# Kernel tuning notes

Hardware: AMD Instinct MI355X
Metric: run time of the kernel (lower is better)

## Reference

```python
import jax, jax.numpy as jnp
import numpy as np

B, L, H, D = 8, 4800, 8, 64  # L = 60*80 tokens, D = head_dim = self.dim


def setup_inputs() -> dict:
    key = jax.random.key(0)
    ks = jax.random.split(key, 8)
    q = jax.random.normal(ks[0], (B, L, H, D), jnp.float32)
    k = jax.random.normal(ks[1], (B, L, H, D), jnp.float32)
    v = jax.random.normal(ks[2], (B, L, H, D), jnp.float32)
    temperature = jnp.ones((H, 1, 1), jnp.float32)          # nn.Parameter(torch.ones(H,1,1))
    attns = jnp.ones((4,), jnp.float32)                      # four scalar gate params (init 1.0)
    # Conv1d(dim,1,k=1): weight [1, dim, 1] -> store as [dim]; bias [1]
    row_w = 0.1 * jax.random.normal(ks[3], (D,), jnp.float32)
    row_b = 0.1 * jax.random.normal(ks[4], (1,), jnp.float32)
    col_w = 0.1 * jax.random.normal(ks[5], (D,), jnp.float32)
    col_b = 0.1 * jax.random.normal(ks[6], (1,), jnp.float32)
    return {"q": q, "k": k, "v": v, "temperature": temperature, "attns": attns,
            "row_w": row_w, "row_b": row_b, "col_w": col_w, "col_b": col_b}


def _l2norm(x):
    # torch F.normalize(dim=-1): x / max(||x||, eps)
    n = jnp.sqrt(jnp.sum(x * x, axis=-1, keepdims=True))
    return x / jnp.maximum(n, 1e-12)


def reference(q, k, v, temperature, attns, row_w, row_b, col_w, col_b):
    # [B,L,H,D] -> [B,H,D,L]
    qt = _l2norm(q.transpose(0, 2, 3, 1))
    kt = _l2norm(k.transpose(0, 2, 3, 1))
    vt = v.transpose(0, 2, 3, 1)
    # channel attention: [B,H,D,D]
    attn = jnp.einsum('bhdl,bhel->bhde', qt, kt)
    # col_conv: Conv1d over C1 rows -> gate per column; row_conv: over C2 -> gate per row
    w_col = jax.nn.sigmoid(jnp.einsum('bhce,c->bhe', attn, col_w) + col_b)[:, :, None, :]  # [B,H,1,C]
    w_row = jax.nn.sigmoid(jnp.einsum('bhce,e->bhc', attn, row_w) + row_b)[:, :, :, None]  # [B,H,C,1]
    attn = (attn * w_col + attn * w_row) * temperature[None]  # temperature [H,1,1] broadcasts
    C = attn.shape[-1]
    neg_inf = jnp.array(-jnp.inf, attn.dtype)
    out = jnp.zeros_like(vt)  # [B,H,D,L]
    for i, tk in enumerate([C // 2, (2 * C) // 3, (3 * C) // 4, (4 * C) // 5]):
        thr = jax.lax.top_k(attn, tk)[0][..., -1:]           # kth largest per row
        a = jnp.where(attn >= thr, attn, neg_inf)            # keep top-k entries
        a = jax.nn.softmax(a, axis=-1)
        out = out + attns[i] * jnp.einsum('bhde,bhel->bhdl', a, vt)
    # rearrange 'b head c (h w) -> b (head c) h w' then back to [B, L, head, c]
    return out.transpose(0, 3, 1, 2)  # [B,L,H,D]
```

## Files before the change

kernel.cpp:

```cpp
#include <hip/hip_runtime.h>

#define B_ 8
#define L_ 4800
#define H_ 8
#define D_ 64
#define BH_ 64

__global__ __launch_bounds__(256) void gram_kernel(
    const float* __restrict__ q, const float* __restrict__ k,
    float* __restrict__ Gp, float* __restrict__ qsqp, float* __restrict__ ksqp,
    const int P, const int NS)
{
  const int p  = blockIdx.x;
  const int b  = blockIdx.y;
  const int hg = blockIdx.z;
  const int t = threadIdx.x;
  const int w = t >> 6, lane = t & 63;
  const int r0 = (lane >> 3) * 8;
  const int c0 = (lane & 7) * 8;

  __shared__ float Ls[2][2][4][8][64];

  const int row  = t >> 6;
  const int col  = lane * 4;
  const int head = lane >> 4;
  const int hc   = (t & 15) * 4;

  const float* qb = q + ((size_t)b * L_ + (size_t)p * NS * 8) * 512 + hg * 256;
  const float* kb = k + ((size_t)b * L_ + (size_t)p * NS * 8) * 512 + hg * 256;
  const size_t off0 = (size_t)row * 512 + col;
  const size_t off1 = off0 + 4 * 512;

  float accG[8][8] = {};
  float sqq0=0.f,sqq1=0.f,sqq2=0.f,sqq3=0.f;
  float sqk0=0.f,sqk1=0.f,sqk2=0.f,sqk3=0.f;

  {
    float4 a0 = *(const float4*)(qb + off0);
    float4 a1 = *(const float4*)(qb + off1);
    float4 b0 = *(const float4*)(kb + off0);
    float4 b1 = *(const float4*)(kb + off1);
    sqq0 += a0.x*a0.x; sqq1 += a0.y*a0.y; sqq2 += a0.z*a0.z; sqq3 += a0.w*a0.w;
    sqq0 += a1.x*a1.x; sqq1 += a1.y*a1.y; sqq2 += a1.z*a1.z; sqq3 += a1.w*a1.w;
    sqk0 += b0.x*b0.x; sqk1 += b0.y*b0.y; sqk2 += b0.z*b0.z; sqk3 += b0.w*b0.w;
    sqk0 += b1.x*b1.x; sqk1 += b1.y*b1.y; sqk2 += b1.z*b1.z; sqk3 += b1.w*b1.w;
    *(float4*)&Ls[0][0][head][row    ][hc] = a0;
    *(float4*)&Ls[0][0][head][row + 4][hc] = a1;
    *(float4*)&Ls[0][1][head][row    ][hc] = b0;
    *(float4*)&Ls[0][1][head][row + 4][hc] = b1;
  }
  __syncthreads();

  for (int s = 0; s < NS; s++) {
    const int cur = s & 1;
    float4 a0, a1, b0, b1;
    const bool pf = (s + 1 < NS);
    if (pf) {
      const float* qp = qb + (size_t)(s + 1) * 4096;
      const float* kp = kb + (size_t)(s + 1) * 4096;
      a0 = *(const float4*)(qp + off0);
      a1 = *(const float4*)(qp + off1);
      b0 = *(const float4*)(kp + off0);
      b1 = *(const float4*)(kp + off1);
    }
    const float (*Lq)[64] = Ls[cur][0][w];
    const float (*Lk)[64] = Ls[cur][1][w];
#pragma unroll
    for (int r = 0; r < 8; r++) {
      float4 qa0 = *(const float4*)&Lq[r][r0];
      float4 qa1 = *(const float4*)&Lq[r][r0 + 4];
      float4 kb0 = *(const float4*)&Lk[r][c0];
      float4 kb1 = *(const float4*)&Lk[r][c0 + 4];
      float av[8] = {qa0.x,qa0.y,qa0.z,qa0.w,qa1.x,qa1.y,qa1.z,qa1.w};
      float bv[8] = {kb0.x,kb0.y,kb0.z,kb0.w,kb1.x,kb1.y,kb1.z,kb1.w};
#pragma unroll
      for (int i = 0; i < 8; i++)
#pragma unroll
        for (int j = 0; j < 8; j++)
          accG[i][j] = fmaf(av[i], bv[j], accG[i][j]);
    }
    if (pf) {
      sqq0 += a0.x*a0.x; sqq1 += a0.y*a0.y; sqq2 += a0.z*a0.z; sqq3 += a0.w*a0.w;
      sqq0 += a1.x*a1.x; sqq1 += a1.y*a1.y; sqq2 += a1.z*a1.z; sqq3 += a1.w*a1.w;
      sqk0 += b0.x*b0.x; sqk1 += b0.y*b0.y; sqk2 += b0.z*b0.z; sqk3 += b0.w*b0.w;
      sqk0 += b1.x*b1.x; sqk1 += b1.y*b1.y; sqk2 += b1.z*b1.z; sqk3 += b1.w*b1.w;
      *(float4*)&Ls[cur ^ 1][0][head][row    ][hc] = a0;
      *(float4*)&Ls[cur ^ 1][0][head][row + 4][hc] = a1;
      *(float4*)&Ls[cur ^ 1][1][head][row    ][hc] = b0;
      *(float4*)&Ls[cur ^ 1][1][head][row + 4][hc] = b1;
    }
    __syncthreads();
  }

  float* gout = Gp + ((size_t)(b * 8 + hg * 4 + w) * P + p) * 4096;
#pragma unroll
  for (int i = 0; i < 8; i++) {
    *(float4*)(gout + (r0 + i) * 64 + c0) =
        make_float4(accG[i][0], accG[i][1], accG[i][2], accG[i][3]);
    *(float4*)(gout + (r0 + i) * 64 + c0 + 4) =
        make_float4(accG[i][4], accG[i][5], accG[i][6], accG[i][7]);
  }

  __syncthreads();
  float4* S4 = (float4*)&Ls[0][0][0][0][0];
  S4[t]       = make_float4(sqq0, sqq1, sqq2, sqq3);
  S4[256 + t] = make_float4(sqk0, sqk1, sqk2, sqk3);
  __syncthreads();
  if (t < 128) {
    const int tensor = t >> 6;
    const int ln = t & 63;
    const float4* Sb = S4 + tensor * 256;
    float4 s0 = Sb[ln], s1 = Sb[64 + ln], s2 = Sb[128 + ln], s3 = Sb[192 + ln];
    float4 r = make_float4(s0.x + s1.x + s2.x + s3.x,
                           s0.y + s1.y + s2.y + s3.y,
                           s0.z + s1.z + s2.z + s3.z,
                           s0.w + s1.w + s2.w + s3.w);
    const int hd = ln >> 4;
    const int dd = (ln & 15) * 4;
    float* dst = tensor ? ksqp : qsqp;
    *(float4*)(dst + ((size_t)(b * 8 + hg * 4 + hd) * P + p) * 64 + dd) = r;
  }
}

__global__ __launch_bounds__(128) void reduce_kernel(
    const float* __restrict__ Gp, const float* __restrict__ qsqp,
    const float* __restrict__ ksqp, float* __restrict__ Gt,
    float* __restrict__ qst, float* __restrict__ kst, const int P)
{
  const int j8 = blockIdx.x;
  const int bh = blockIdx.y;
  const int t = threadIdx.x;
  const size_t off = (size_t)j8 * 512 + (size_t)t * 4;
  const float* gp = Gp + (size_t)bh * P * 4096 + off;

  float4 a0 = make_float4(0.f,0.f,0.f,0.f);
  float4 a1 = make_float4(0.f,0.f,0.f,0.f);
  float4 a2 = make_float4(0.f,0.f,0.f,0.f);
  float4 a3 = make_float4(0.f,0.f,0.f,0.f);
  int p = 0;
  for (; p + 4 <= P; p += 4) {
    float4 g0 = *(const float4*)(gp + (size_t)(p + 0) * 4096);
    float4 g1 = *(const float4*)(gp + (size_t)(p + 1) * 4096);
    float4 g2 = *(const float4*)(gp + (size_t)(p + 2) * 4096);
    float4 g3 = *(const float4*)(gp + (size_t)(p + 3) * 4096);
    a0.x += g0.x; a0.y += g0.y; a0.z += g0.z; a0.w += g0.w;
    a1.x += g1.x; a1.y += g1.y; a1.z += g1.z; a1.w += g1.w;
    a2.x += g2.x; a2.y += g2.y; a2.z += g2.z; a2.w += g2.w;
    a3.x += g3.x; a3.y += g3.y; a3.z += g3.z; a3.w += g3.w;
  }
  for (; p < P; p++) {
    float4 g = *(const float4*)(gp + (size_t)p * 4096);
    a0.x += g.x; a0.y += g.y; a0.z += g.z; a0.w += g.w;
  }
  float4 r = make_float4(a0.x + a1.x + a2.x + a3.x,
                         a0.y + a1.y + a2.y + a3.y,
                         a0.z + a1.z + a2.z + a3.z,
                         a0.w + a1.w + a2.w + a3.w);
  *(float4*)(Gt + (size_t)bh * 4096 + off) = r;

  if (j8 == 0) {
    const int d2 = t & 63;
    const float* sp = (t < 64) ? qsqp : ksqp;
    const float* s = sp + (size_t)bh * P * 64 + d2;
    float x0 = 0.f, x1 = 0.f, x2 = 0.f, x3 = 0.f;
    int pp = 0;
    for (; pp + 4 <= P; pp += 4) {
      x0 += s[(size_t)(pp + 0) * 64];
      x1 += s[(size_t)(pp + 1) * 64];
      x2 += s[(size_t)(pp + 2) * 64];
      x3 += s[(size_t)(pp + 3) * 64];
    }
    for (; pp < P; pp++) x0 += s[(size_t)pp * 64];
    float* dst = (t < 64) ? qst : kst;
    dst[bh * 64 + d2] = x0 + x1 + x2 + x3;
  }
}

__global__ __launch_bounds__(256) void mask_kernel(
    const float* __restrict__ Gt, const float* __restrict__ qst,
    const float* __restrict__ kst,
    const float* __restrict__ temperature, const float* __restrict__ attns,
    const float* __restrict__ row_w, const float* __restrict__ row_b,
    const float* __restrict__ col_w, const float* __restrict__ col_b,
    float* __restrict__ Mt)
{
  const int bh = blockIdx.x;
  const int h = bh & 7;
  const int t = threadIdx.x;
  const int d = t & 63, q4 = t >> 6;
  const int e0 = q4 * 16;

  __shared__ float att[64][65];
  __shared__ float rnq[64], rnk[64], cw[64], rw[64];
  __shared__ float wcol[64], wrow[64];
  __shared__ float thr[4][64];
  __shared__ float pmax[4][64];
  __shared__ float rowmax[64];
  __shared__ float psum[4][4][64];
  __shared__ float rinv[4][64];

  if (t < 64) {
    rnq[t] = 1.0f / fmaxf(sqrtf(qst[bh * 64 + t]), 1e-12f);
  } else if (t < 128) {
    rnk[t - 64] = 1.0f / fmaxf(sqrtf(kst[bh * 64 + (t - 64)]), 1e-12f);
  } else if (t < 192) {
    cw[t - 128] = col_w[t - 128];
  } else {
    rw[t - 192] = row_w[t - 192];
  }
  __syncthreads();

  {
    const float rq = rnq[d];
#pragma unroll
    for (int ee = 0; ee < 16; ee += 4) {
      float4 g = *(const float4*)&Gt[(size_t)bh * 4096 + d * 64 + e0 + ee];
      att[d][e0+ee+0] = g.x * rq * rnk[e0+ee+0];
      att[d][e0+ee+1] = g.y * rq * rnk[e0+ee+1];
      att[d][e0+ee+2] = g.z * rq * rnk[e0+ee+2];
      att[d][e0+ee+3] = g.w * rq * rnk[e0+ee+3];
    }
  }
  __syncthreads();

  if (t < 64) {
    float s = 0.f;
    for (int c = 0; c < 64; c++) s += att[c][t] * cw[c];
    s += col_b[0];
    wcol[t] = 1.0f / (1.0f + __expf(-s));
  } else if (t < 128) {
    int c = t - 64;
    float s = 0.f;
    for (int e = 0; e < 64; e++) s += att[c][e] * rw[e];
    s += row_b[0];
    wrow[c] = 1.0f / (1.0f + __expf(-s));
  }
  __syncthreads();

  {
    const float temp = temperature[h];
    const float wr = wrow[d];
    float mx = -1e30f;
#pragma unroll
    for (int ee = 0; ee < 16; ee++) {
      float x = att[d][e0+ee] * ((wcol[e0+ee] + wr) * temp);
      att[d][e0+ee] = x;
      mx = fmaxf(mx, x);
    }
    pmax[q4][d] = mx;
  }
  __syncthreads();
  if (t < 64)
    rowmax[t] = fmaxf(fmaxf(pmax[0][t], pmax[1][t]), fmaxf(pmax[2][t], pmax[3][t]));

  {
    float x[16];
#pragma unroll
    for (int j = 0; j < 16; j++) x[j] = att[d][e0+j];
    int gt[16] = {}, ge[16] = {};
    for (int m = 0; m < 64; m++) {
      float y = att[d][m];
#pragma unroll
      for (int j = 0; j < 16; j++) { gt[j] += (y > x[j]); ge[j] += (y >= x[j]); }
    }
    const int tks[4] = {32, 42, 48, 51};
#pragma unroll
    for (int j = 0; j < 16; j++)
#pragma unroll
      for (int i = 0; i < 4; i++)
        if (gt[j] <= tks[i]-1 && ge[j] >= tks[i]) thr[i][d] = x[j];
  }
  __syncthreads();

  {
    const float rm = rowmax[d];
    const float t0 = thr[0][d], t1 = thr[1][d], t2 = thr[2][d], t3 = thr[3][d];
    float s0=0.f, s1=0.f, s2=0.f, s3=0.f;
#pragma unroll
    for (int ee = 0; ee < 16; ee++) {
      float xv = att[d][e0+ee];
      float ex = __expf(xv - rm);
      if (xv >= t0) s0 += ex;
      if (xv >= t1) s1 += ex;
      if (xv >= t2) s2 += ex;
      if (xv >= t3) s3 += ex;
    }
    psum[q4][0][d] = s0; psum[q4][1][d] = s1; psum[q4][2][d] = s2; psum[q4][3][d] = s3;
  }
  __syncthreads();
  if (t < 64) {
#pragma unroll
    for (int i = 0; i < 4; i++) {
      float s = psum[0][i][t] + psum[1][i][t] + psum[2][i][t] + psum[3][i][t];
      rinv[i][t] = attns[i] / s;
    }
  }
  __syncthreads();

  {
    const float rm = rowmax[d];
    const float t0 = thr[0][d], t1 = thr[1][d], t2 = thr[2][d], t3 = thr[3][d];
    const float r0 = rinv[0][d], r1 = rinv[1][d], r2 = rinv[2][d], r3 = rinv[3][d];
    float* mo = Mt + (size_t)bh * 4096;
#pragma unroll
    for (int ee = 0; ee < 16; ee++) {
      float xv = att[d][e0+ee];
      float ex = __expf(xv - rm);
      float m = 0.f;
      if (xv >= t0) m += r0 * ex;
      if (xv >= t1) m += r1 * ex;
      if (xv >= t2) m += r2 * ex;
      if (xv >= t3) m += r3 * ex;
      mo[(e0 + ee) * 64 + d] = m;
    }
  }
}

__global__ __launch_bounds__(64, 2) void apply_kernel(
    const float* __restrict__ Mt, const float* __restrict__ v,
    float* __restrict__ out)
{
  const int bh = blockIdx.y;
  const int b = bh >> 3, h = bh & 7;
  const int l0 = blockIdx.x * 64;
  const int lane = threadIdx.x;

  __shared__ float Vs[64][68];

  const int tg  = lane >> 4;
  const int e0w = (lane & 15) * 4;
#pragma unroll
  for (int it = 0; it < 16; it++) {
    const int tl = it * 4 + tg;
    float4 x = *(const float4*)(v + (((size_t)b * L_ + l0 + tl) * 8 + h) * 64 + e0w);
    const int cs = e0w ^ ((tl >> 3) << 2);
    *(float4*)&Vs[tl][cs] = x;
  }
  __syncthreads();

  const int dg = lane >> 3, lg = lane & 7;
  const int d0 = dg * 8;
  float acc[8][8] = {};
  const float* Mtb = Mt + (size_t)bh * 4096;

  for (int e = 0; e < 64; e += 4) {
    float mt[4][8];
#pragma unroll
    for (int j = 0; j < 4; j++) {
      float4 m0 = *(const float4*)(Mtb + (e + j) * 64 + d0);
      float4 m1 = *(const float4*)(Mtb + (e + j) * 64 + d0 + 4);
      mt[j][0]=m0.x; mt[j][1]=m0.y; mt[j][2]=m0.z; mt[j][3]=m0.w;
      mt[j][4]=m1.x; mt[j][5]=m1.y; mt[j][6]=m1.z; mt[j][7]=m1.w;
    }
#pragma unroll
    for (int jj = 0; jj < 8; jj++) {
      const int tl = lg * 8 + jj;
      const int cs = e ^ (lg << 2);
      float4 vv = *(const float4*)&Vs[tl][cs];
#pragma unroll
      for (int i = 0; i < 8; i++) {
        acc[jj][i] = fmaf(mt[0][i], vv.x, acc[jj][i]);
        acc[jj][i] = fmaf(mt[1][i], vv.y, acc[jj][i]);
        acc[jj][i] = fmaf(mt[2][i], vv.z, acc[jj][i]);
        acc[jj][i] = fmaf(mt[3][i], vv.w, acc[jj][i]);
      }
    }
  }

#pragma unroll
  for (int jj = 0; jj < 8; jj++) {
    const int tl = lg * 8 + jj;
    float* orow = out + (((size_t)b * L_ + l0 + tl) * 8 + h) * 64 + d0;
    *(float4*)(orow)     = make_float4(acc[jj][0], acc[jj][1], acc[jj][2], acc[jj][3]);
    *(float4*)(orow + 4) = make_float4(acc[jj][4], acc[jj][5], acc[jj][6], acc[jj][7]);
  }
}

extern "C" void kernel_launch(void* const* d_in, const int* in_sizes, int n_in,
                              void* d_out, int out_size, void* d_ws, size_t ws_size,
                              hipStream_t stream) {
  const float* q           = (const float*)d_in[0];
  const float* k           = (const float*)d_in[1];
  const float* v           = (const float*)d_in[2];
  const float* temperature = (const float*)d_in[3];
  const float* attns       = (const float*)d_in[4];
  const float* row_w       = (const float*)d_in[5];
  const float* row_b       = (const float*)d_in[6];
  const float* col_w       = (const float*)d_in[7];
  const float* col_b       = (const float*)d_in[8];
  float* out = (float*)d_out;

  auto needB = [](long long P) -> size_t {
    return (size_t)(270336LL * P + 532480LL) * 4u;
  };
  int P = 60;
  if (ws_size < needB(60)) P = 30;
  if (ws_size < needB(30)) P = 15;
  const int NS = 600 / P;

  float* ws = (float*)d_ws;
  const size_t GPs = (size_t)64 * P * 4096;
  const size_t SQs = (size_t)64 * P * 64;
  float* Gp   = ws;
  float* qsqp = Gp + GPs;
  float* ksqp = qsqp + SQs;
  float* Gt   = ksqp + SQs;
  float* qst  = Gt + 262144;
  float* kst  = qst + 4096;
  float* Mt   = kst + 4096;

  gram_kernel<<<dim3(P, B_, 2), 256, 0, stream>>>(q, k, Gp, qsqp, ksqp, P, NS);
  reduce_kernel<<<dim3(8, BH_), 128, 0, stream>>>(Gp, qsqp, ksqp, Gt, qst, kst, P);
  mask_kernel<<<dim3(BH_), 256, 0, stream>>>(Gt, qst, kst, temperature, attns,
                                             row_w, row_b, col_w, col_b, Mt);
  apply_kernel<<<dim3(L_ / 64, BH_), 64, 0, stream>>>(Mt, v, out);
}
```

Baseline: 339.5 us.

## Drop LDS staging in gram and apply kernels, use per-thread row outer products

The gram kernel no longer double-buffers q/k tiles in shared memory. Each wavefront now owns one (batch·head, chunk) pair and reads its rows directly from global memory into registers, with the chunk count changed to 48 so each chunk covers 100 rows. The apply kernel gives each thread one token and all 64 output channels, reading the 64×64 mask matrix from global/cache and holding 64 accumulators. This removes LDS traffic and block-wide barriers, but adds redundant global loads of q/k across lanes and per-thread matrix reads, plus higher register pressure in apply.

```diff
diff --git a/kernel.cpp b/kernel.cpp
--- a/kernel.cpp
+++ b/kernel.cpp
@@ -9,90 +9,46 @@
 __global__ __launch_bounds__(256) void gram_kernel(
     const float* __restrict__ q, const float* __restrict__ k,
     float* __restrict__ Gp, float* __restrict__ qsqp, float* __restrict__ ksqp,
-    const int P, const int NS)
+    const int P, const int CL)
 {
-  const int p  = blockIdx.x;
-  const int b  = blockIdx.y;
-  const int hg = blockIdx.z;
   const int t = threadIdx.x;
   const int w = t >> 6, lane = t & 63;
+  const int wid = blockIdx.x * 4 + w;
+  const int bh = wid / P;
+  const int p  = wid - bh * P;
+  const int b = bh >> 3, h = bh & 7;
   const int r0 = (lane >> 3) * 8;
   const int c0 = (lane & 7) * 8;
 
-  __shared__ float Ls[2][2][4][8][64];
-
-  const int row  = t >> 6;
-  const int col  = lane * 4;
-  const int head = lane >> 4;
-  const int hc   = (t & 15) * 4;
-
-  const float* qb = q + ((size_t)b * L_ + (size_t)p * NS * 8) * 512 + hg * 256;
-  const float* kb = k + ((size_t)b * L_ + (size_t)p * NS * 8) * 512 + hg * 256;
-  const size_t off0 = (size_t)row * 512 + col;
-  const size_t off1 = off0 + 4 * 512;
+  const float* qb = q + ((size_t)b * L_ + (size_t)p * CL) * 512 + h * 64;
+  const float* kb = k + ((size_t)b * L_ + (size_t)p * CL) * 512 + h * 64;
 
   float accG[8][8] = {};
-  float sqq0=0.f,sqq1=0.f,sqq2=0.f,sqq3=0.f;
-  float sqk0=0.f,sqk1=0.f,sqk2=0.f,sqk3=0.f;
-
-  {
-    float4 a0 = *(const float4*)(qb + off0);
-    float4 a1 = *(const float4*)(qb + off1);
-    float4 b0 = *(const float4*)(kb + off0);
-    float4 b1 = *(const float4*)(kb + off1);
-    sqq0 += a0.x*a0.x; sqq1 += a0.y*a0.y; sqq2 += a0.z*a0.z; sqq3 += a0.w*a0.w;
-    sqq0 += a1.x*a1.x; sqq1 += a1.y*a1.y; sqq2 += a1.z*a1.z; sqq3 += a1.w*a1.w;
-    sqk0 += b0.x*b0.x; sqk1 += b0.y*b0.y; sqk2 += b0.z*b0.z; sqk3 += b0.w*b0.w;
-    sqk0 += b1.x*b1.x; sqk1 += b1.y*b1.y; sqk2 += b1.z*b1.z; sqk3 += b1.w*b1.w;
-    *(float4*)&Ls[0][0][head][row    ][hc] = a0;
-    *(float4*)&Ls[0][0][head][row + 4][hc] = a1;
-    *(float4*)&Ls[0][1][head][row    ][hc] = b0;
-    *(float4*)&Ls[0][1][head][row + 4][hc] = b1;
-  }
-  __syncthreads();
-
-  for (int s = 0; s < NS; s++) {
-    const int cur = s & 1;
-    float4 a0, a1, b0, b1;
-    const bool pf = (s + 1 < NS);
-    if (pf) {
-      const float* qp = qb + (size_t)(s + 1) * 4096;
-      const float* kp = kb + (size_t)(s + 1) * 4096;
-      a0 = *(const float4*)(qp + off0);
-      a1 = *(const float4*)(qp + off1);
-      b0 = *(const float4*)(kp + off0);
-      b1 = *(const float4*)(kp + off1);
-    }
-    const float (*Lq)[64] = Ls[cur][0][w];
-    const float (*Lk)[64] = Ls[cur][1][w];
-#pragma unroll
-    for (int r = 0; r < 8; r++) {
-      float4 qa0 = *(const float4*)&Lq[r][r0];
-      float4 qa1 = *(const float4*)&Lq[r][r0 + 4];
-      float4 kb0 = *(const float4*)&Lk[r][c0];
-      float4 kb1 = *(const float4*)&Lk[r][c0 + 4];
-      float av[8] = {qa0.x,qa0.y,qa0.z,qa0.w,qa1.x,qa1.y,qa1.z,qa1.w};
-      float bv[8] = {kb0.x,kb0.y,kb0.z,kb0.w,kb1.x,kb1.y,kb1.z,kb1.w};
-#pragma unroll
-      for (int i = 0; i < 8; i++)
-#pragma unroll
-        for (int j = 0; j < 8; j++)
-          accG[i][j] = fmaf(av[i], bv[j], accG[i][j]);
-    }
-    if (pf) {
-      sqq0 += a0.x*a0.x; sqq1 += a0.y*a0.y; sqq2 += a0.z*a0.z; sqq3 += a0.w*a0.w;
-      sqq0 += a1.x*a1.x; sqq1 += a1.y*a1.y; sqq2 += a1.z*a1.z; sqq3 += a1.w*a1.w;
-      sqk0 += b0.x*b0.x; sqk1 += b0.y*b0.y; sqk2 += b0.z*b0.z; sqk3 += b0.w*b0.w;
-      sqk0 += b1.x*b1.x; sqk1 += b1.y*b1.y; sqk2 += b1.z*b1.z; sqk3 += b1.w*b1.w;
-      *(float4*)&Ls[cur ^ 1][0][head][row    ][hc] = a0;
-      *(float4*)&Ls[cur ^ 1][0][head][row + 4][hc] = a1;
-      *(float4*)&Ls[cur ^ 1][1][head][row    ][hc] = b0;
-      *(float4*)&Ls[cur ^ 1][1][head][row + 4][hc] = b1;
-    }
-    __syncthreads();
-  }
-
-  float* gout = Gp + ((size_t)(b * 8 + hg * 4 + w) * P + p) * 4096;
+  float sqq[8] = {0,0,0,0,0,0,0,0};
+  float sqk[8] = {0,0,0,0,0,0,0,0};
+
+#pragma unroll 2
+  for (int r = 0; r < CL; ++r) {
+    const float* qr = qb + (size_t)r * 512;
+    const float* kr = kb + (size_t)r * 512;
+    float4 qa0 = *(const float4*)(qr + r0);
+    float4 qa1 = *(const float4*)(qr + r0 + 4);
+    float4 kv0 = *(const float4*)(kr + c0);
+    float4 kv1 = *(const float4*)(kr + c0 + 4);
+    float av[8] = {qa0.x,qa0.y,qa0.z,qa0.w,qa1.x,qa1.y,qa1.z,qa1.w};
+    float bv[8] = {kv0.x,kv0.y,kv0.z,kv0.w,kv1.x,kv1.y,kv1.z,kv1.w};
+#pragma unroll
+    for (int i = 0; i < 8; i++)
+#pragma unroll
+      for (int j = 0; j < 8; j++)
+        accG[i][j] = fmaf(av[i], bv[j], accG[i][j]);
+#pragma unroll
+    for (int j = 0; j < 8; j++) sqq[j] = fmaf(av[j], av[j], sqq[j]);
+#pragma unroll
+    for (int j = 0; j < 8; j++) sqk[j] = fmaf(bv[j], bv[j], sqk[j]);
+  }
+
+  float* gout = Gp + ((size_t)bh * P + p) * 4096;
 #pragma unroll
   for (int i = 0; i < 8; i++) {
     *(float4*)(gout + (r0 + i) * 64 + c0) =
@@ -101,25 +57,18 @@
         make_float4(accG[i][4], accG[i][5], accG[i][6], accG[i][7]);
   }
 
-  __syncthreads();
-  float4* S4 = (float4*)&Ls[0][0][0][0][0];
-  S4[t]       = make_float4(sqq0, sqq1, sqq2, sqq3);
-  S4[256 + t] = make_float4(sqk0, sqk1, sqk2, sqk3);
-  __syncthreads();
-  if (t < 128) {
-    const int tensor = t >> 6;
-    const int ln = t & 63;
-    const float4* Sb = S4 + tensor * 256;
-    float4 s0 = Sb[ln], s1 = Sb[64 + ln], s2 = Sb[128 + ln], s3 = Sb[192 + ln];
-    float4 r = make_float4(s0.x + s1.x + s2.x + s3.x,
-                           s0.y + s1.y + s2.y + s3.y,
-                           s0.z + s1.z + s2.z + s3.z,
-                           s0.w + s1.w + s2.w + s3.w);
-    const int hd = ln >> 4;
-    const int dd = (ln & 15) * 4;
-    float* dst = tensor ? ksqp : qsqp;
-    *(float4*)(dst + ((size_t)(b * 8 + hg * 4 + hd) * P + p) * 64 + dd) = r;
-  }
+  __shared__ float sqs[4][2][64];
+  if ((lane & 7) == 0) {
+#pragma unroll
+    for (int j = 0; j < 8; j++) sqs[w][0][r0 + j] = sqq[j];
+  }
+  if (lane < 8) {
+#pragma unroll
+    for (int j = 0; j < 8; j++) sqs[w][1][c0 + j] = sqk[j];
+  }
+  __syncthreads();
+  qsqp[((size_t)bh * P + p) * 64 + lane] = sqs[w][0][lane];
+  ksqp[((size_t)bh * P + p) * 64 + lane] = sqs[w][1][lane];
 }
 
 __global__ __launch_bounds__(128) void reduce_kernel(
@@ -316,63 +265,44 @@
   }
 }
 
-__global__ __launch_bounds__(64, 2) void apply_kernel(
+__global__ __launch_bounds__(256) void apply_kernel(
     const float* __restrict__ Mt, const float* __restrict__ v,
     float* __restrict__ out)
 {
   const int bh = blockIdx.y;
   const int b = bh >> 3, h = bh & 7;
-  const int l0 = blockIdx.x * 64;
-  const int lane = threadIdx.x;
-
-  __shared__ float Vs[64][68];
-
-  const int tg  = lane >> 4;
-  const int e0w = (lane & 15) * 4;
-#pragma unroll
-  for (int it = 0; it < 16; it++) {
-    const int tl = it * 4 + tg;
-    float4 x = *(const float4*)(v + (((size_t)b * L_ + l0 + tl) * 8 + h) * 64 + e0w);
-    const int cs = e0w ^ ((tl >> 3) << 2);
-    *(float4*)&Vs[tl][cs] = x;
-  }
-  __syncthreads();
-
-  const int dg = lane >> 3, lg = lane & 7;
-  const int d0 = dg * 8;
-  float acc[8][8] = {};
-  const float* Mtb = Mt + (size_t)bh * 4096;
-
-  for (int e = 0; e < 64; e += 4) {
-    float mt[4][8];
-#pragma unroll
-    for (int j = 0; j < 4; j++) {
-      float4 m0 = *(const float4*)(Mtb + (e + j) * 64 + d0);
-      float4 m1 = *(const float4*)(Mtb + (e + j) * 64 + d0 + 4);
-      mt[j][0]=m0.x; mt[j][1]=m0.y; mt[j][2]=m0.z; mt[j][3]=m0.w;
-      mt[j][4]=m1.x; mt[j][5]=m1.y; mt[j][6]=m1.z; mt[j][7]=m1.w;
-    }
-#pragma unroll
-    for (int jj = 0; jj < 8; jj++) {
-      const int tl = lg * 8 + jj;
-      const int cs = e ^ (lg << 2);
-      float4 vv = *(const float4*)&Vs[tl][cs];
-#pragma unroll
-      for (int i = 0; i < 8; i++) {
-        acc[jj][i] = fmaf(mt[0][i], vv.x, acc[jj][i]);
-        acc[jj][i] = fmaf(mt[1][i], vv.y, acc[jj][i]);
-        acc[jj][i] = fmaf(mt[2][i], vv.z, acc[jj][i]);
-        acc[jj][i] = fmaf(mt[3][i], vv.w, acc[jj][i]);
+  const int l = blockIdx.x * 256 + threadIdx.x;
+  const bool ok = (l < L_);
+  const float* __restrict__ Mb = Mt + (size_t)bh * 4096;
+  const float* vrow = v + (((size_t)b * L_ + (size_t)(ok ? l : 0)) * 8 + h) * 64;
+
+  float acc[64];
+#pragma unroll
+  for (int d = 0; d < 64; d++) acc[d] = 0.f;
+
+  for (int e4 = 0; e4 < 16; ++e4) {
+    float4 vv = *(const float4*)(vrow + e4 * 4);
+#pragma unroll
+    for (int j = 0; j < 4; ++j) {
+      const float4* mr = (const float4*)(Mb + (e4 * 4 + j) * 64);
+      const float vj = (j == 0) ? vv.x : (j == 1) ? vv.y : (j == 2) ? vv.z : vv.w;
+#pragma unroll
+      for (int d4 = 0; d4 < 16; ++d4) {
+        float4 m = mr[d4];
+        acc[d4*4+0] = fmaf(m.x, vj, acc[d4*4+0]);
+        acc[d4*4+1] = fmaf(m.y, vj, acc[d4*4+1]);
+        acc[d4*4+2] = fmaf(m.z, vj, acc[d4*4+2]);
+        acc[d4*4+3] = fmaf(m.w, vj, acc[d4*4+3]);
       }
     }
   }
 
-#pragma unroll
-  for (int jj = 0; jj < 8; jj++) {
-    const int tl = lg * 8 + jj;
-    float* orow = out + (((size_t)b * L_ + l0 + tl) * 8 + h) * 64 + d0;
-    *(float4*)(orow)     = make_float4(acc[jj][0], acc[jj][1], acc[jj][2], acc[jj][3]);
-    *(float4*)(orow + 4) = make_float4(acc[jj][4], acc[jj][5], acc[jj][6], acc[jj][7]);
+  if (ok) {
+    float* orow = out + (((size_t)b * L_ + l) * 8 + h) * 64;
+#pragma unroll
+    for (int d4 = 0; d4 < 16; ++d4)
+      *(float4*)(orow + d4 * 4) =
+          make_float4(acc[d4*4+0], acc[d4*4+1], acc[d4*4+2], acc[d4*4+3]);
   }
 }
 
@@ -393,10 +323,10 @@
   auto needB = [](long long P) -> size_t {
     return (size_t)(270336LL * P + 532480LL) * 4u;
   };
-  int P = 60;
-  if (ws_size < needB(60)) P = 30;
-  if (ws_size < needB(30)) P = 15;
-  const int NS = 600 / P;
+  int P = 48;
+  if (ws_size < needB(48)) P = 24;
+  if (ws_size < needB(24)) P = 12;
+  const int CL = L_ / P;
 
   float* ws = (float*)d_ws;
   const size_t GPs = (size_t)64 * P * 4096;
@@ -409,9 +339,9 @@
   float* kst  = qst + 4096;
   float* Mt   = kst + 4096;
 
-  gram_kernel<<<dim3(P, B_, 2), 256, 0, stream>>>(q, k, Gp, qsqp, ksqp, P, NS);
+  gram_kernel<<<dim3(16 * P, 1), 256, 0, stream>>>(q, k, Gp, qsqp, ksqp, P, CL);
   reduce_kernel<<<dim3(8, BH_), 128, 0, stream>>>(Gp, qsqp, ksqp, Gt, qst, kst, P);
   mask_kernel<<<dim3(BH_), 256, 0, stream>>>(Gt, qst, kst, temperature, attns,
                                              row_w, row_b, col_w, col_b, Mt);
-  apply_kernel<<<dim3(L_ / 64, BH_), 64, 0, stream>>>(Mt, v, out);
-}
+  apply_kernel<<<dim3((L_ + 255) / 256, BH_), 256, 0, stream>>>(Mt, v, out);
+}
```

After: 392.5 us. 15.6% more time.

## Restructure Gram kernel: one head per block, per-wave L-chunks, in-block reduction

Applied to the files above, without the earlier changes.

The Gram kernel now gives each block a single (batch, head) pair and a contiguous L chunk. Each of the four waves streams its own 8-row slices through private double-buffered shared memory, which removes the per-iteration block-wide __syncthreads. The four wave partial Gram matrices are summed in shared memory before being written, so fewer partials (P=30 instead of 60) reach the reduce kernel and global traffic drops. In exchange, each q/k load now reads only 256 B per row per head (less coalesced than the old 1 KB rows), and the grid is smaller.

```diff
diff --git a/kernel.cpp b/kernel.cpp
--- a/kernel.cpp
+++ b/kernel.cpp
@@ -11,66 +11,64 @@
     float* __restrict__ Gp, float* __restrict__ qsqp, float* __restrict__ ksqp,
     const int P, const int NS)
 {
-  const int p  = blockIdx.x;
-  const int b  = blockIdx.y;
-  const int hg = blockIdx.z;
+  const int bh = blockIdx.y;
+  const int b = bh >> 3, h = bh & 7;
+  const int cx = blockIdx.x;
+  const int l0 = cx * (NS * 32);
   const int t = threadIdx.x;
   const int w = t >> 6, lane = t & 63;
+
+  __shared__ float Ls[4][2][2][8][64];
+
+  const int lrow = lane >> 4;
+  const int lcol = (lane & 15) * 4;
   const int r0 = (lane >> 3) * 8;
   const int c0 = (lane & 7) * 8;
 
-  __shared__ float Ls[2][2][4][8][64];
-
-  const int row  = t >> 6;
-  const int col  = lane * 4;
-  const int head = lane >> 4;
-  const int hc   = (t & 15) * 4;
-
-  const float* qb = q + ((size_t)b * L_ + (size_t)p * NS * 8) * 512 + hg * 256;
-  const float* kb = k + ((size_t)b * L_ + (size_t)p * NS * 8) * 512 + hg * 256;
-  const size_t off0 = (size_t)row * 512 + col;
-  const size_t off1 = off0 + 4 * 512;
+  const float* qb = q + (size_t)(b*L_)*512 + h*64;
+  const float* kb = k + (size_t)(b*L_)*512 + h*64;
 
   float accG[8][8] = {};
-  float sqq0=0.f,sqq1=0.f,sqq2=0.f,sqq3=0.f;
-  float sqk0=0.f,sqk1=0.f,sqk2=0.f,sqk3=0.f;
-
-  {
-    float4 a0 = *(const float4*)(qb + off0);
-    float4 a1 = *(const float4*)(qb + off1);
-    float4 b0 = *(const float4*)(kb + off0);
-    float4 b1 = *(const float4*)(kb + off1);
-    sqq0 += a0.x*a0.x; sqq1 += a0.y*a0.y; sqq2 += a0.z*a0.z; sqq3 += a0.w*a0.w;
-    sqq0 += a1.x*a1.x; sqq1 += a1.y*a1.y; sqq2 += a1.z*a1.z; sqq3 += a1.w*a1.w;
-    sqk0 += b0.x*b0.x; sqk1 += b0.y*b0.y; sqk2 += b0.z*b0.z; sqk3 += b0.w*b0.w;
-    sqk0 += b1.x*b1.x; sqk1 += b1.y*b1.y; sqk2 += b1.z*b1.z; sqk3 += b1.w*b1.w;
-    *(float4*)&Ls[0][0][head][row    ][hc] = a0;
-    *(float4*)&Ls[0][0][head][row + 4][hc] = a1;
-    *(float4*)&Ls[0][1][head][row    ][hc] = b0;
-    *(float4*)&Ls[0][1][head][row + 4][hc] = b1;
-  }
-  __syncthreads();
+  float sqq[4] = {0,0,0,0}, sqk[4] = {0,0,0,0};
+
+  {
+    const int ls = l0 + w*8;
+    const float* qp = qb + (size_t)(ls + lrow)*512 + lcol;
+    const float* kp = kb + (size_t)(ls + lrow)*512 + lcol;
+    float4 a0 = *(const float4*)qp;
+    float4 a1 = *(const float4*)(qp + 4*512);
+    float4 b0 = *(const float4*)kp;
+    float4 b1 = *(const float4*)(kp + 4*512);
+    sqq[0]+=a0.x*a0.x; sqq[1]+=a0.y*a0.y; sqq[2]+=a0.z*a0.z; sqq[3]+=a0.w*a0.w;
+    sqq[0]+=a1.x*a1.x; sqq[1]+=a1.y*a1.y; sqq[2]+=a1.z*a1.z; sqq[3]+=a1.w*a1.w;
+    sqk[0]+=b0.x*b0.x; sqk[1]+=b0.y*b0.y; sqk[2]+=b0.z*b0.z; sqk[3]+=b0.w*b0.w;
+    sqk[0]+=b1.x*b1.x; sqk[1]+=b1.y*b1.y; sqk[2]+=b1.z*b1.z; sqk[3]+=b1.w*b1.w;
+    *(float4*)&Ls[w][0][0][lrow  ][lcol] = a0;
+    *(float4*)&Ls[w][0][0][lrow+4][lcol] = a1;
+    *(float4*)&Ls[w][0][1][lrow  ][lcol] = b0;
+    *(float4*)&Ls[w][0][1][lrow+4][lcol] = b1;
+  }
 
   for (int s = 0; s < NS; s++) {
     const int cur = s & 1;
     float4 a0, a1, b0, b1;
-    const bool pf = (s + 1 < NS);
-    if (pf) {
-      const float* qp = qb + (size_t)(s + 1) * 4096;
-      const float* kp = kb + (size_t)(s + 1) * 4096;
-      a0 = *(const float4*)(qp + off0);
-      a1 = *(const float4*)(qp + off1);
-      b0 = *(const float4*)(kp + off0);
-      b1 = *(const float4*)(kp + off1);
-    }
-    const float (*Lq)[64] = Ls[cur][0][w];
-    const float (*Lk)[64] = Ls[cur][1][w];
+    if (s + 1 < NS) {
+      const int ls = l0 + (w + 4*(s+1))*8;
+      const float* qp = qb + (size_t)(ls + lrow)*512 + lcol;
+      const float* kp = kb + (size_t)(ls + lrow)*512 + lcol;
+      a0 = *(const float4*)qp;
+      a1 = *(const float4*)(qp + 4*512);
+      b0 = *(const float4*)kp;
+      b1 = *(const float4*)(kp + 4*512);
+    }
+    const float (*Lq)[64] = Ls[w][cur][0];
+    const float (*Lk)[64] = Ls[w][cur][1];
 #pragma unroll
     for (int r = 0; r < 8; r++) {
       float4 qa0 = *(const float4*)&Lq[r][r0];
-      float4 qa1 = *(const float4*)&Lq[r][r0 + 4];
+      float4 qa1 = *(const float4*)&Lq[r][r0+4];
       float4 kb0 = *(const float4*)&Lk[r][c0];
-      float4 kb1 = *(const float4*)&Lk[r][c0 + 4];
+      float4 kb1 = *(const float4*)&Lk[r][c0+4];
       float av[8] = {qa0.x,qa0.y,qa0.z,qa0.w,qa1.x,qa1.y,qa1.z,qa1.w};
       float bv[8] = {kb0.x,kb0.y,kb0.z,kb0.w,kb1.x,kb1.y,kb1.z,kb1.w};
 #pragma unroll
@@ -79,46 +77,72 @@
         for (int j = 0; j < 8; j++)
           accG[i][j] = fmaf(av[i], bv[j], accG[i][j]);
     }
-    if (pf) {
-      sqq0 += a0.x*a0.x; sqq1 += a0.y*a0.y; sqq2 += a0.z*a0.z; sqq3 += a0.w*a0.w;
-      sqq0 += a1.x*a1.x; sqq1 += a1.y*a1.y; sqq2 += a1.z*a1.z; sqq3 += a1.w*a1.w;
-      sqk0 += b0.x*b0.x; sqk1 += b0.y*b0.y; sqk2 += b0.z*b0.z; sqk3 += b0.w*b0.w;
-      sqk0 += b1.x*b1.x; sqk1 += b1.y*b1.y; sqk2 += b1.z*b1.z; sqk3 += b1.w*b1.w;
-      *(float4*)&Ls[cur ^ 1][0][head][row    ][hc] = a0;
-      *(float4*)&Ls[cur ^ 1][0][head][row + 4][hc] = a1;
-      *(float4*)&Ls[cur ^ 1][1][head][row    ][hc] = b0;
-      *(float4*)&Ls[cur ^ 1][1][head][row + 4][hc] = b1;
-    }
-    __syncthreads();
-  }
-
-  float* gout = Gp + ((size_t)(b * 8 + hg * 4 + w) * P + p) * 4096;
-#pragma unroll
-  for (int i = 0; i < 8; i++) {
-    *(float4*)(gout + (r0 + i) * 64 + c0) =
-        make_float4(accG[i][0], accG[i][1], accG[i][2], accG[i][3]);
-    *(float4*)(gout + (r0 + i) * 64 + c0 + 4) =
-        make_float4(accG[i][4], accG[i][5], accG[i][6], accG[i][7]);
-  }
-
-  __syncthreads();
-  float4* S4 = (float4*)&Ls[0][0][0][0][0];
-  S4[t]       = make_float4(sqq0, sqq1, sqq2, sqq3);
-  S4[256 + t] = make_float4(sqk0, sqk1, sqk2, sqk3);
+    if (s + 1 < NS) {
+      sqq[0]+=a0.x*a0.x; sqq[1]+=a0.y*a0.y; sqq[2]+=a0.z*a0.z; sqq[3]+=a0.w*a0.w;
+      sqq[0]+=a1.x*a1.x; sqq[1]+=a1.y*a1.y; sqq[2]+=a1.z*a1.z; sqq[3]+=a1.w*a1.w;
+      sqk[0]+=b0.x*b0.x; sqk[1]+=b0.y*b0.y; sqk[2]+=b0.z*b0.z; sqk[3]+=b0.w*b0.w;
+      sqk[0]+=b1.x*b1.x; sqk[1]+=b1.y*b1.y; sqk[2]+=b1.z*b1.z; sqk[3]+=b1.w*b1.w;
+      *(float4*)&Ls[w][cur^1][0][lrow  ][lcol] = a0;
+      *(float4*)&Ls[w][cur^1][0][lrow+4][lcol] = a1;
+      *(float4*)&Ls[w][cur^1][1][lrow  ][lcol] = b0;
+      *(float4*)&Ls[w][cur^1][1][lrow+4][lcol] = b1;
+    }
+  }
+
+  float* red = &Ls[0][0][0][0][0];
+  float4* redf4 = (float4*)red;
+  float* gout = Gp + ((size_t)bh*P + cx)*4096;
+
+  __syncthreads();
+  if (r0 < 32) {
+#pragma unroll
+    for (int i = 0; i < 8; i++) {
+      *(float4*)&red[w*2048 + (r0+i)*64 + c0    ] = make_float4(accG[i][0],accG[i][1],accG[i][2],accG[i][3]);
+      *(float4*)&red[w*2048 + (r0+i)*64 + c0 + 4] = make_float4(accG[i][4],accG[i][5],accG[i][6],accG[i][7]);
+    }
+  }
+  __syncthreads();
+#pragma unroll
+  for (int pp = 0; pp < 2; pp++) {
+    int fi = t + pp*256;
+    float4 s0 = redf4[fi], s1 = redf4[512+fi], s2 = redf4[1024+fi], s3 = redf4[1536+fi];
+    float4 r; r.x = s0.x+s1.x+s2.x+s3.x; r.y = s0.y+s1.y+s2.y+s3.y;
+    r.z = s0.z+s1.z+s2.z+s3.z; r.w = s0.w+s1.w+s2.w+s3.w;
+    *(float4*)&gout[fi*4] = r;
+  }
+  __syncthreads();
+  if (r0 >= 32) {
+#pragma unroll
+    for (int i = 0; i < 8; i++) {
+      *(float4*)&red[w*2048 + (r0-32+i)*64 + c0    ] = make_float4(accG[i][0],accG[i][1],accG[i][2],accG[i][3]);
+      *(float4*)&red[w*2048 + (r0-32+i)*64 + c0 + 4] = make_float4(accG[i][4],accG[i][5],accG[i][6],accG[i][7]);
+    }
+  }
+  __syncthreads();
+#pragma unroll
+  for (int pp = 0; pp < 2; pp++) {
+    int fi = t + pp*256;
+    float4 s0 = redf4[fi], s1 = redf4[512+fi], s2 = redf4[1024+fi], s3 = redf4[1536+fi];
+    float4 r; r.x = s0.x+s1.x+s2.x+s3.x; r.y = s0.y+s1.y+s2.y+s3.y;
+    r.z = s0.z+s1.z+s2.z+s3.z; r.w = s0.w+s1.w+s2.w+s3.w;
+    *(float4*)&gout[2048 + fi*4] = r;
+  }
+  __syncthreads();
+  redf4[w*64 + lane]       = make_float4(sqq[0],sqq[1],sqq[2],sqq[3]);
+  redf4[256 + w*64 + lane] = make_float4(sqk[0],sqk[1],sqk[2],sqk[3]);
   __syncthreads();
   if (t < 128) {
-    const int tensor = t >> 6;
-    const int ln = t & 63;
-    const float4* Sb = S4 + tensor * 256;
-    float4 s0 = Sb[ln], s1 = Sb[64 + ln], s2 = Sb[128 + ln], s3 = Sb[192 + ln];
-    float4 r = make_float4(s0.x + s1.x + s2.x + s3.x,
-                           s0.y + s1.y + s2.y + s3.y,
-                           s0.z + s1.z + s2.z + s3.z,
-                           s0.w + s1.w + s2.w + s3.w);
-    const int hd = ln >> 4;
-    const int dd = (ln & 15) * 4;
-    float* dst = tensor ? ksqp : qsqp;
-    *(float4*)(dst + ((size_t)(b * 8 + hg * 4 + hd) * P + p) * 64 + dd) = r;
+    const int d = t & 63;
+    const int col4 = d >> 2, c = d & 3;
+    const int base = (t < 64) ? 0 : 1024;
+    float s = 0.f;
+#pragma unroll
+    for (int ww = 0; ww < 4; ww++)
+#pragma unroll
+      for (int m = 0; m < 4; m++)
+        s += red[base + (ww*64 + m*16 + col4)*4 + c];
+    float* dst = (t < 64) ? qsqp : ksqp;
+    dst[((size_t)bh*P + cx)*64 + d] = s;
   }
 }
 
@@ -393,10 +417,9 @@
   auto needB = [](long long P) -> size_t {
     return (size_t)(270336LL * P + 532480LL) * 4u;
   };
-  int P = 60;
-  if (ws_size < needB(60)) P = 30;
+  int P = 30;
   if (ws_size < needB(30)) P = 15;
-  const int NS = 600 / P;
+  const int NS = L_ / (P * 32);
 
   float* ws = (float*)d_ws;
   const size_t GPs = (size_t)64 * P * 4096;
@@ -409,7 +432,7 @@
   float* kst  = qst + 4096;
   float* Mt   = kst + 4096;
 
-  gram_kernel<<<dim3(P, B_, 2), 256, 0, stream>>>(q, k, Gp, qsqp, ksqp, P, NS);
+  gram_kernel<<<dim3(P, BH_), 256, 0, stream>>>(q, k, Gp, qsqp, ksqp, P, NS);
   reduce_kernel<<<dim3(8, BH_), 128, 0, stream>>>(Gp, qsqp, ksqp, Gt, qst, kst, P);
   mask_kernel<<<dim3(BH_), 256, 0, stream>>>(Gt, qst, kst, temperature, attns,
                                              row_w, row_b, col_w, col_b, Mt);
```

After: 326.9 us. 3.7% less time.
